# Performance work log

Hardware: AMD Instinct MI355X
Metric: run time of the kernel (lower is better)

The kernel has to match this reference:

```python
import jax, jax.numpy as jnp
import numpy as np

B, N, D, K = 16, 1024, 512, 16  # batch graphs, nodes/graph, feat dim, knn k
NEG_SLOPE = 0.2


def setup_inputs() -> dict:
    key = jax.random.key(0)
    ks = jax.random.split(key, 16)
    s = 1.0 / np.sqrt(D)
    p = {}
    p["x"] = jax.random.normal(ks[0], (B, N, D), dtype=jnp.float32)
    for i, l in enumerate(["1", "2", "3"]):
        p["W" + l] = jax.random.normal(ks[1 + 4 * i], (D, D), dtype=jnp.float32) * s
        p["asrc" + l] = jax.random.normal(ks[2 + 4 * i], (D,), dtype=jnp.float32) * s
        p["adst" + l] = jax.random.normal(ks[3 + 4 * i], (D,), dtype=jnp.float32) * s
        p["b" + l] = jnp.zeros((D,), dtype=jnp.float32)
    p["Wc"] = jax.random.normal(ks[13], (D, 2), dtype=jnp.float32) * s
    p["bc"] = jnp.zeros((2,), dtype=jnp.float32)
    return p


def _knn_idx(pos):
    # pos: [N, D]. k nearest neighbors by euclidean distance, self excluded
    sq = jnp.sum(pos * pos, axis=1)
    d2 = sq[:, None] + sq[None, :] - 2.0 * (pos @ pos.T)  # [N, N]
    d2 = jnp.where(jnp.eye(N, dtype=bool), jnp.inf, d2)
    _, idx = jax.lax.top_k(-d2, K)  # [N, K] neighbor (source) indices per node
    return idx


def _normalize_scale(pos):
    # PyG NormalizeScale: center, then scale so max abs coord ~ 1
    pos = pos - pos.mean(axis=0, keepdims=True)
    return pos * (0.999999 / jnp.max(jnp.abs(pos)))


def _gat(h, nbr, W, asrc, adst, b):
    # GATConv, 1 head, self-loops already included in nbr [N, K+1]
    hp = h @ W                                   # [N, D]
    a_s = hp @ asrc                              # [N] att for sources
    a_d = hp @ adst                              # [N] att for targets
    e = jax.nn.leaky_relu(a_s[nbr] + a_d[:, None], NEG_SLOPE)  # [N, K+1]
    att = jax.nn.softmax(e, axis=-1)             # softmax over each node's in-edges
    msg = hp[nbr]                                # [N, K+1, D] gathered neighbor feats
    return jnp.einsum('nk,nkd->nd', att, msg) + b


def reference(x, W1, asrc1, adst1, b1, W2, asrc2, adst2, b2, W3, asrc3, adst3, b3, Wc, bc):
    self_idx = jnp.arange(N)[:, None]

    def per_graph(pos):
        nbr = jnp.concatenate([_knn_idx(pos), self_idx], axis=1)  # [N, K+1] w/ self-loop
        h = _normalize_scale(pos)
        h = jax.nn.relu(_gat(h, nbr, W1, asrc1, adst1, b1))
        h = jax.nn.relu(_gat(h, nbr, W2, asrc2, adst2, b2))
        h = _gat(h, nbr, W3, asrc3, adst3, b3)
        return h.max(axis=0)  # global max pool over nodes

    g = jax.vmap(per_graph)(x)  # [B, D]
    return g @ Wc + bc          # [B, 2]
```

## Files before the change

### kernel.cpp

```cpp
#include <hip/hip_runtime.h>
#include <hip/hip_bf16.h>
#include <math.h>

#define BATCH 16
#define NNODE 1024
#define DIM   512
#define KNN   16
#define KP1   17
#define NCAND 20
#define NEG   0.2f
#define BT    128
#define NCH   16

typedef __attribute__((ext_vector_type(8))) short bf16x8;
typedef __attribute__((ext_vector_type(4))) float f32x4;

__device__ __forceinline__ unsigned short f2bf(float f) {
    unsigned u = __float_as_uint(f);
    unsigned r = (u + 0x7FFFu + ((u >> 16) & 1u)) >> 16;
    return (unsigned short)r;
}
__device__ __forceinline__ float bf2f(unsigned short h) {
    return __uint_as_float(((unsigned)h) << 16);
}
__device__ __forceinline__ void split_store(float v, unsigned short* hi, unsigned short* lo, size_t idx) {
    unsigned short h = f2bf(v);
    hi[idx] = h;
    lo[idx] = f2bf(v - bf2f(h));
}

__global__ __launch_bounds__(256) void colmean_part(const float* __restrict__ x, float* __restrict__ part) {
    int b = blockIdx.x, dc = blockIdx.y, ch = blockIdx.z;
    int d = dc * 256 + threadIdx.x;
    const float* p = x + ((size_t)b * NNODE + ch * (NNODE / NCH)) * DIM + d;
    float s = 0.f;
    #pragma unroll 4
    for (int n = 0; n < NNODE / NCH; ++n) s += p[(size_t)n * DIM];
    part[((size_t)b * NCH + ch) * DIM + d] = s;
}
__global__ void colmean_fin(const float* __restrict__ part, float* __restrict__ mean) {
    int id = blockIdx.x * 256 + threadIdx.x;
    int b = id >> 9, d = id & (DIM - 1);
    float s = 0.f;
    #pragma unroll
    for (int ch = 0; ch < NCH; ++ch) s += part[((size_t)b * NCH + ch) * DIM + d];
    mean[id] = s * (1.0f / NNODE);
}

__global__ void rowsq_kernel(const float* __restrict__ x, float* __restrict__ sq) {
    int row = blockIdx.x * 4 + (threadIdx.x >> 6);
    int lane = threadIdx.x & 63;
    const float* p = x + (size_t)row * DIM;
    float s = 0.f;
    for (int i = lane; i < DIM; i += 64) { float v = p[i]; s += v * v; }
    #pragma unroll
    for (int off = 32; off > 0; off >>= 1) s += __shfl_down(s, off, 64);
    if (lane == 0) sq[row] = s;
}

__global__ void xtobf_kernel(const float* __restrict__ x, unsigned short* __restrict__ xh) {
    int id = blockIdx.x * 256 + threadIdx.x;
    float4 v = *(const float4*)(x + (size_t)id * 4);
    ushort4 o;
    o.x = f2bf(v.x); o.y = f2bf(v.y); o.z = f2bf(v.z); o.w = f2bf(v.w);
    *(ushort4*)(xh + (size_t)id * 4) = o;
}

__global__ __launch_bounds__(256, 2) void dist_mfma(const unsigned short* __restrict__ xh,
                                                    const float* __restrict__ sq,
                                                    float* __restrict__ d2) {
    __shared__ unsigned short AhL[128][40], BhL[128][40];
    int mt = blockIdx.y;
    int b = mt >> 3;
    int m0 = mt * BT;
    int n0 = blockIdx.x * BT;
    int bn0 = b * NNODE + n0;
    int t = threadIdx.x;
    int lane = t & 63, w = t >> 6;
    int wm = (w >> 1) * 64, wn = (w & 1) * 64;
    int fr = lane & 15, fk = (lane >> 4) * 8;
    f32x4 acc[4][4];
    #pragma unroll
    for (int i = 0; i < 4; ++i)
        #pragma unroll
        for (int j = 0; j < 4; ++j) acc[i][j] = (f32x4){0.f, 0.f, 0.f, 0.f};

    for (int k0 = 0; k0 < DIM; k0 += 32) {
        if (k0) __syncthreads();
        #pragma unroll
        for (int p = 0; p < 2; ++p) {
            int u = t + p * 256;
            int row = u >> 2, seg = (u & 3) * 8;
            *(uint4*)&AhL[row][seg] = *(const uint4*)(xh + (size_t)(m0 + row) * DIM + k0 + seg);
            *(uint4*)&BhL[row][seg] = *(const uint4*)(xh + (size_t)(bn0 + row) * DIM + k0 + seg);
        }
        __syncthreads();
        bf16x8 ah[4], bh[4];
        #pragma unroll
        for (int i = 0; i < 4; ++i) {
            ah[i] = *(const bf16x8*)&AhL[wm + i * 16 + fr][fk];
            bh[i] = *(const bf16x8*)&BhL[wn + i * 16 + fr][fk];
        }
        #pragma unroll
        for (int i = 0; i < 4; ++i)
            #pragma unroll
            for (int j = 0; j < 4; ++j)
                acc[i][j] = __builtin_amdgcn_mfma_f32_16x16x32_bf16(ah[i], bh[j], acc[i][j], 0, 0, 0);
    }
    const float* sqb = sq + b * NNODE;
    int mloc0 = m0 - b * NNODE;
    #pragma unroll
    for (int i = 0; i < 4; ++i) {
        int mloc = mloc0 + wm + i * 16 + (lane >> 4) * 4;
        #pragma unroll
        for (int j = 0; j < 4; ++j) {
            int n = n0 + wn + j * 16 + fr;
            float sqn = sqb[n];
            #pragma unroll
            for (int r = 0; r < 4; ++r) {
                float val = sqb[mloc + r] + sqn - 2.f * acc[i][j][r];
                if (mloc + r == n) val = INFINITY;
                d2[((size_t)b * NNODE + mloc + r) * NNODE + n] = val;
            }
        }
    }
}

__global__ __launch_bounds__(256) void knn_kernel(const float* __restrict__ d2, int* __restrict__ cand) {
    int row = blockIdx.x * 4 + (threadIdx.x >> 6);
    int l = threadIdx.x & 63;
    const float* src = d2 + (size_t)row * NNODE;
    unsigned key[16];
    #pragma unroll
    for (int j = 0; j < 16; ++j) {
        unsigned v = __float_as_uint(src[l + (j << 6)]);
        key[j] = (v & 0xFFFFFC00u) | (unsigned)(l + (j << 6));
    }
    int* dst = cand + row * NCAND;
    unsigned T = 0;
    for (int it = 0; it < NCAND; ++it) {
        unsigned lmin = 0xFFFFFFFFu;
        #pragma unroll
        for (int j = 0; j < 16; ++j) {
            unsigned k = (key[j] > T) ? key[j] : 0xFFFFFFFFu;
            lmin = min(lmin, k);
        }
        #pragma unroll
        for (int off = 1; off < 64; off <<= 1) {
            unsigned o = (unsigned)__shfl_xor((int)lmin, off, 64);
            lmin = min(lmin, o);
        }
        T = lmin;
        if (l == 0) dst[it] = (int)(lmin & 1023u);
    }
}

__global__ __launch_bounds__(256) void rerank_kernel(const float* __restrict__ x,
                                                     const float* __restrict__ sq,
                                                     const int* __restrict__ cand,
                                                     int* __restrict__ nbr) {
    int bid = blockIdx.x;
    int b = bid & (BATCH - 1);
    int w = threadIdx.x >> 6, l = threadIdx.x & 63;
    int m = (bid >> 4) * 4 + w;
    int row = b * NNODE + m;
    const float* xb = x + (size_t)b * NNODE * DIM;
    const float* sqb = sq + b * NNODE;
    const float* xm = xb + (size_t)m * DIM;
    float4 m0v = *(const float4*)(xm + l * 8);
    float4 m1v = *(const float4*)(xm + l * 8 + 4);
    float sqm = sqb[m];

    int idx[NCAND];
    #pragma unroll
    for (int c = 0; c < NCAND; ++c) idx[c] = cand[row * NCAND + c];

    float s[NCAND];
    #pragma unroll
    for (int half = 0; half < 2; ++half) {
        float4 j0[10], j1[10];
        #pragma unroll
        for (int i = 0; i < 10; ++i) {
            const float* xj = xb + (size_t)idx[half * 10 + i] * DIM;
            j0[i] = *(const float4*)(xj + l * 8);
            j1[i] = *(const float4*)(xj + l * 8 + 4);
        }
        #pragma unroll
        for (int i = 0; i < 10; ++i)
            s[half * 10 + i] = m0v.x * j0[i].x + m0v.y * j0[i].y + m0v.z * j0[i].z + m0v.w * j0[i].w
                             + m1v.x * j1[i].x + m1v.y * j1[i].y + m1v.z * j1[i].z + m1v.w * j1[i].w;
    }
    #pragma unroll
    for (int off = 32; off > 0; off >>= 1)
        #pragma unroll
        for (int c = 0; c < NCAND; ++c) s[c] += __shfl_xor(s[c], off, 64);

    unsigned long long key[NCAND];
    #pragma unroll
    for (int c = 0; c < NCAND; ++c) {
        float dv = sqm + sqb[idx[c]] - 2.f * s[c];
        key[c] = ((unsigned long long)__float_as_uint(dv) << 32) | (unsigned)idx[c];
    }
    unsigned long long mykey = ~0ull;
    int myidx = 0;
    #pragma unroll
    for (int c = 0; c < NCAND; ++c) {
        if (l == c) { mykey = key[c]; myidx = idx[c]; }
    }
    int rank = 0;
    #pragma unroll
    for (int c = 0; c < NCAND; ++c) rank += (key[c] < mykey) ? 1 : 0;

    int* dst = nbr + row * KP1;
    if (l < NCAND && rank < KNN) dst[rank] = myidx;
    if (l == 0) dst[KNN] = m;
}

__global__ void init_maxabs(unsigned* maxabs) { if (threadIdx.x < BATCH) maxabs[threadIdx.x] = 0u; }

__global__ __launch_bounds__(256) void maxabs_kernel(const float* __restrict__ x,
                                                     const float* __restrict__ mean,
                                                     unsigned* __restrict__ maxabs) {
    int b = blockIdx.y;
    const float* p = x + ((size_t)b * NNODE + blockIdx.x * 64) * DIM;
    const float* mb = mean + b * DIM;
    float m = 0.f;
    for (int i = threadIdx.x; i < 64 * DIM; i += 256) {
        int d = i & (DIM - 1);
        m = fmaxf(m, fabsf(p[i] - mb[d]));
    }
    __shared__ float red[256];
    red[threadIdx.x] = m; __syncthreads();
    for (int s = 128; s > 0; s >>= 1) {
        if (threadIdx.x < s) red[threadIdx.x] = fmaxf(red[threadIdx.x], red[threadIdx.x + s]);
        __syncthreads();
    }
    if (threadIdx.x == 0) atomicMax(maxabs + b, __float_as_uint(red[0]));
}

__global__ void normalize_kernel(const float* __restrict__ x, const float* __restrict__ mean,
                                 const unsigned* __restrict__ maxabs,
                                 unsigned short* __restrict__ h_hi, unsigned short* __restrict__ h_lo) {
    int id = blockIdx.x * 256 + threadIdx.x;
    int b = id >> 19;
    int d = id & (DIM - 1);
    float scale = 0.999999f / __uint_as_float(maxabs[b]);
    float v = (x[id] - mean[b * DIM + d]) * scale;
    split_store(v, h_hi, h_lo, id);
}

__global__ void wsplit_kernel(const float* __restrict__ W,
                              unsigned short* __restrict__ Wh, unsigned short* __restrict__ Wl) {
    __shared__ float tile[32][33];
    int bx = blockIdx.x * 32, by = blockIdx.y * 32;
    int tx = threadIdx.x & 31, ty = threadIdx.x >> 5;
    #pragma unroll
    for (int i = 0; i < 4; ++i)
        tile[ty + i * 8][tx] = W[(size_t)(by + ty + i * 8) * DIM + bx + tx];
    __syncthreads();
    #pragma unroll
    for (int i = 0; i < 4; ++i) {
        int n = bx + ty + i * 8;
        float v = tile[tx][ty + i * 8];
        split_store(v, Wh, Wl, (size_t)n * DIM + by + tx);
    }
}

__global__ __launch_bounds__(256, 2) void gemm_mfma(const unsigned short* __restrict__ Agh,
                                                    const unsigned short* __restrict__ Agl,
                                                    const unsigned short* __restrict__ Bgh,
                                                    const unsigned short* __restrict__ Bgl,
                                                    float* __restrict__ C) {
    __shared__ unsigned short AhL[128][40], AlL[128][40], BhL[128][40], BlL[128][40];
    int m0 = blockIdx.y * BT, n0 = blockIdx.x * BT;
    int t = threadIdx.x;
    int lane = t & 63, w = t >> 6;
    int wm = (w >> 1) * 64, wn = (w & 1) * 64;
    int fr = lane & 15, fk = (lane >> 4) * 8;
    f32x4 acc[4][4];
    #pragma unroll
    for (int i = 0; i < 4; ++i)
        #pragma unroll
        for (int j = 0; j < 4; ++j) acc[i][j] = (f32x4){0.f, 0.f, 0.f, 0.f};

    for (int k0 = 0; k0 < DIM; k0 += 32) {
        if (k0) __syncthreads();
        #pragma unroll
        for (int p = 0; p < 2; ++p) {
            int u = t + p * 256;
            int row = u >> 2, seg = (u & 3) * 8;
            *(uint4*)&AhL[row][seg] = *(const uint4*)(Agh + (size_t)(m0 + row) * DIM + k0 + seg);
            *(uint4*)&AlL[row][seg] = *(const uint4*)(Agl + (size_t)(m0 + row) * DIM + k0 + seg);
            *(uint4*)&BhL[row][seg] = *(const uint4*)(Bgh + (size_t)(n0 + row) * DIM + k0 + seg);
            *(uint4*)&BlL[row][seg] = *(const uint4*)(Bgl + (size_t)(n0 + row) * DIM + k0 + seg);
        }
        __syncthreads();
        bf16x8 ah[4], al[4], bh[4], bl[4];
        #pragma unroll
        for (int i = 0; i < 4; ++i) {
            ah[i] = *(const bf16x8*)&AhL[wm + i * 16 + fr][fk];
            al[i] = *(const bf16x8*)&AlL[wm + i * 16 + fr][fk];
            bh[i] = *(const bf16x8*)&BhL[wn + i * 16 + fr][fk];
            bl[i] = *(const bf16x8*)&BlL[wn + i * 16 + fr][fk];
        }
        #pragma unroll
        for (int i = 0; i < 4; ++i)
            #pragma unroll
            for (int j = 0; j < 4; ++j) {
                acc[i][j] = __builtin_amdgcn_mfma_f32_16x16x32_bf16(ah[i], bh[j], acc[i][j], 0, 0, 0);
                acc[i][j] = __builtin_amdgcn_mfma_f32_16x16x32_bf16(ah[i], bl[j], acc[i][j], 0, 0, 0);
                acc[i][j] = __builtin_amdgcn_mfma_f32_16x16x32_bf16(al[i], bh[j], acc[i][j], 0, 0, 0);
            }
    }
    #pragma unroll
    for (int i = 0; i < 4; ++i) {
        int mrow = m0 + wm + i * 16 + (lane >> 4) * 4;
        #pragma unroll
        for (int j = 0; j < 4; ++j) {
            int col = n0 + wn + j * 16 + fr;
            #pragma unroll
            for (int r = 0; r < 4; ++r)
                C[(size_t)(mrow + r) * DIM + col] = acc[i][j][r];
        }
    }
}

__global__ void attvec_kernel(const float* __restrict__ hp, const float* __restrict__ asrc,
                              const float* __restrict__ adst, float* __restrict__ as_,
                              float* __restrict__ ad_) {
    int row = blockIdx.x * 4 + (threadIdx.x >> 6);
    int lane = threadIdx.x & 63;
    const float4* p = (const float4*)(hp + (size_t)row * DIM);
    const float4* s4 = (const float4*)asrc;
    const float4* d4 = (const float4*)adst;
    float4 a0 = p[lane], a1 = p[lane + 64];
    float4 u0 = s4[lane], u1 = s4[lane + 64];
    float4 v0 = d4[lane], v1 = d4[lane + 64];
    float s = a0.x * u0.x + a0.y * u0.y + a0.z * u0.z + a0.w * u0.w
            + a1.x * u1.x + a1.y * u1.y + a1.z * u1.z + a1.w * u1.w;
    float d = a0.x * v0.x + a0.y * v0.y + a0.z * v0.z + a0.w * v0.w
            + a1.x * v1.x + a1.y * v1.y + a1.z * v1.z + a1.w * v1.w;
    #pragma unroll
    for (int off = 32; off > 0; off >>= 1) { s += __shfl_down(s, off, 64); d += __shfl_down(d, off, 64); }
    if (lane == 0) { as_[row] = s; ad_[row] = d; }
}

template<int RELU, int SPLIT>
__global__ __launch_bounds__(256) void aggr_kernel(const float* __restrict__ hp, const int* __restrict__ nbr,
                                                   const float* __restrict__ as_, const float* __restrict__ ad_,
                                                   const float* __restrict__ bias,
                                                   float* __restrict__ outf,
                                                   unsigned short* __restrict__ oh,
                                                   unsigned short* __restrict__ ol) {
    __shared__ float attL[4][KP1];
    __shared__ int   jjL[4][KP1];
    int bid = blockIdx.x;
    int b = bid & (BATCH - 1);
    int w = threadIdx.x >> 6, l = threadIdx.x & 63;
    int n = (bid >> 4) * 4 + w;
    int id = b * NNODE + n;

    float e = -INFINITY;
    if (l < KP1) {
        int j = nbr[id * KP1 + l];
        jjL[w][l] = j;
        e = as_[b * NNODE + j] + ad_[id];
        e = (e >= 0.f) ? e : NEG * e;
    }
    float mx = e;
    #pragma unroll
    for (int off = 16; off > 0; off >>= 1) mx = fmaxf(mx, __shfl_xor(mx, off, 64));
    float ex = (l < KP1) ? expf(e - mx) : 0.f;
    float sm = ex;
    #pragma unroll
    for (int off = 16; off > 0; off >>= 1) sm += __shfl_xor(sm, off, 64);
    if (l < KP1) attL[w][l] = ex / sm;

    const float* base = hp + (size_t)b * NNODE * DIM;
    int d0 = l * 8;
    const float4* b4 = (const float4*)(bias + d0);
    float4 o0 = b4[0], o1 = b4[1];
    #pragma unroll
    for (int k = 0; k < KP1; ++k) {
        float a = attL[w][k];
        const float* vp = base + (size_t)jjL[w][k] * DIM + d0;
        float4 v0 = *(const float4*)vp;
        float4 v1 = *(const float4*)(vp + 4);
        o0.x += a * v0.x; o0.y += a * v0.y; o0.z += a * v0.z; o0.w += a * v0.w;
        o1.x += a * v1.x; o1.y += a * v1.y; o1.z += a * v1.z; o1.w += a * v1.w;
    }
    if (RELU) {
        o0.x = fmaxf(o0.x, 0.f); o0.y = fmaxf(o0.y, 0.f); o0.z = fmaxf(o0.z, 0.f); o0.w = fmaxf(o0.w, 0.f);
        o1.x = fmaxf(o1.x, 0.f); o1.y = fmaxf(o1.y, 0.f); o1.z = fmaxf(o1.z, 0.f); o1.w = fmaxf(o1.w, 0.f);
    }
    size_t idx = (size_t)id * DIM + d0;
    if (SPLIT) {
        float v[8] = {o0.x, o0.y, o0.z, o0.w, o1.x, o1.y, o1.z, o1.w};
        unsigned hi[4], lo[4];
        #pragma unroll
        for (int i = 0; i < 4; ++i) {
            unsigned short h0 = f2bf(v[2 * i]),     h1 = f2bf(v[2 * i + 1]);
            unsigned short l0 = f2bf(v[2 * i] - bf2f(h0));
            unsigned short l1 = f2bf(v[2 * i + 1] - bf2f(h1));
            hi[i] = (unsigned)h0 | ((unsigned)h1 << 16);
            lo[i] = (unsigned)l0 | ((unsigned)l1 << 16);
        }
        *(uint4*)(oh + idx) = *(uint4*)hi;
        *(uint4*)(ol + idx) = *(uint4*)lo;
    } else {
        *(float4*)(outf + idx) = o0;
        *(float4*)(outf + idx + 4) = o1;
    }
}

__global__ __launch_bounds__(256) void maxpool_part(const float* __restrict__ h, float* __restrict__ part) {
    int b = blockIdx.x, dc = blockIdx.y, ch = blockIdx.z;
    int d = dc * 256 + threadIdx.x;
    const float* p = h + ((size_t)b * NNODE + ch * (NNODE / NCH)) * DIM + d;
    float m = -INFINITY;
    #pragma unroll 4
    for (int n = 0; n < NNODE / NCH; ++n) m = fmaxf(m, p[(size_t)n * DIM]);
    part[((size_t)b * NCH + ch) * DIM + d] = m;
}
__global__ void maxpool_fin(const float* __restrict__ part, float* __restrict__ g) {
    int id = blockIdx.x * 256 + threadIdx.x;
    int b = id >> 9, d = id & (DIM - 1);
    float m = -INFINITY;
    #pragma unroll
    for (int ch = 0; ch < NCH; ++ch) m = fmaxf(m, part[((size_t)b * NCH + ch) * DIM + d]);
    g[id] = m;
}

__global__ void final_kernel(const float* __restrict__ g, const float* __restrict__ Wc,
                             const float* __restrict__ bc, float* __restrict__ out) {
    int b = blockIdx.x, t = threadIdx.x;
    float s0 = 0.f, s1 = 0.f;
    for (int d = t; d < DIM; d += 256) {
        float v = g[b * DIM + d];
        s0 += v * Wc[d * 2 + 0];
        s1 += v * Wc[d * 2 + 1];
    }
    __shared__ float r0[256], r1[256];
    r0[t] = s0; r1[t] = s1; __syncthreads();
    for (int s = 128; s > 0; s >>= 1) {
        if (t < s) { r0[t] += r0[t + s]; r1[t] += r1[t + s]; }
        __syncthreads();
    }
    if (t == 0) { out[b * 2] = r0[0] + bc[0]; out[b * 2 + 1] = r1[0] + bc[1]; }
}

extern "C" void kernel_launch(void* const* d_in, const int* in_sizes, int n_in,
                              void* d_out, int out_size, void* d_ws, size_t ws_size,
                              hipStream_t stream) {
    const float* x     = (const float*)d_in[0];
    const float* W1    = (const float*)d_in[1];
    const float* asrc1 = (const float*)d_in[2];
    const float* adst1 = (const float*)d_in[3];
    const float* b1    = (const float*)d_in[4];
    const float* W2    = (const float*)d_in[5];
    const float* asrc2 = (const float*)d_in[6];
    const float* adst2 = (const float*)d_in[7];
    const float* b2    = (const float*)d_in[8];
    const float* W3    = (const float*)d_in[9];
    const float* asrc3 = (const float*)d_in[10];
    const float* adst3 = (const float*)d_in[11];
    const float* b3    = (const float*)d_in[12];
    const float* Wc    = (const float*)d_in[13];
    const float* bc    = (const float*)d_in[14];
    float* out = (float*)d_out;

    char* ws = (char*)d_ws;
    float*          d2    = (float*)ws;
    float*          hp    = (float*)ws;
    unsigned short* hA_hi = (unsigned short*)(ws + (32ull << 20));
    unsigned short* hA_lo = (unsigned short*)(ws + (48ull << 20));
    unsigned short* xh    = (unsigned short*)(ws + (64ull << 20));
    unsigned short* hB_hi = (unsigned short*)(ws + (64ull << 20));
    unsigned short* hB_lo = (unsigned short*)(ws + (80ull << 20));
    float*          h3    = (float*)(ws + (64ull << 20));
    size_t off = 96ull << 20;
    unsigned short* Wt1h = (unsigned short*)(ws + off); off += (size_t)DIM * DIM * 2;
    unsigned short* Wt1l = (unsigned short*)(ws + off); off += (size_t)DIM * DIM * 2;
    unsigned short* Wt2h = (unsigned short*)(ws + off); off += (size_t)DIM * DIM * 2;
    unsigned short* Wt2l = (unsigned short*)(ws + off); off += (size_t)DIM * DIM * 2;
    unsigned short* Wt3h = (unsigned short*)(ws + off); off += (size_t)DIM * DIM * 2;
    unsigned short* Wt3l = (unsigned short*)(ws + off); off += (size_t)DIM * DIM * 2;
    int*      nbr    = (int*)(ws + off);      off += (size_t)BATCH * NNODE * KP1 * 4;
    int*      cand   = (int*)(ws + off);      off += (size_t)BATCH * NNODE * NCAND * 4;
    float*    sq     = (float*)(ws + off);    off += (size_t)BATCH * NNODE * 4;
    float*    mean   = (float*)(ws + off);    off += (size_t)BATCH * DIM * 4;
    unsigned* maxabs = (unsigned*)(ws + off); off += 256;
    float*    as_    = (float*)(ws + off);    off += (size_t)BATCH * NNODE * 4;
    float*    ad_    = (float*)(ws + off);    off += (size_t)BATCH * NNODE * 4;
    float*    g      = (float*)(ws + off);    off += (size_t)BATCH * DIM * 4;
    float*    part   = (float*)(ws + off);    off += (size_t)BATCH * NCH * DIM * 4;
    (void)ws_size; (void)in_sizes; (void)n_in; (void)out_size;

    const dim3 cgrid(BATCH, DIM / 256, NCH);
    colmean_part<<<cgrid, 256, 0, stream>>>(x, part);
    colmean_fin<<<BATCH * DIM / 256, 256, 0, stream>>>(part, mean);
    rowsq_kernel<<<BATCH * NNODE / 4, 256, 0, stream>>>(x, sq);
    xtobf_kernel<<<BATCH * NNODE * DIM / 1024, 256, 0, stream>>>(x, xh);
    dist_mfma<<<dim3(NNODE / BT, BATCH * NNODE / BT), 256, 0, stream>>>(xh, sq, d2);
    knn_kernel<<<BATCH * NNODE / 4, 256, 0, stream>>>(d2, cand);
    rerank_kernel<<<BATCH * NNODE / 4, 256, 0, stream>>>(x, sq, cand, nbr);
    wsplit_kernel<<<dim3(16, 16), 256, 0, stream>>>(W1, Wt1h, Wt1l);
    wsplit_kernel<<<dim3(16, 16), 256, 0, stream>>>(W2, Wt2h, Wt2l);
    wsplit_kernel<<<dim3(16, 16), 256, 0, stream>>>(W3, Wt3h, Wt3l);
    init_maxabs<<<1, 64, 0, stream>>>(maxabs);
    maxabs_kernel<<<dim3(16, BATCH), 256, 0, stream>>>(x, mean, maxabs);
    normalize_kernel<<<BATCH * NNODE * DIM / 256, 256, 0, stream>>>(x, mean, maxabs, hA_hi, hA_lo);

    const dim3 ggrid(DIM / BT, BATCH * NNODE / BT);
    gemm_mfma<<<ggrid, 256, 0, stream>>>(hA_hi, hA_lo, Wt1h, Wt1l, hp);
    attvec_kernel<<<BATCH * NNODE / 4, 256, 0, stream>>>(hp, asrc1, adst1, as_, ad_);
    aggr_kernel<1, 1><<<BATCH * NNODE / 4, 256, 0, stream>>>(hp, nbr, as_, ad_, b1, nullptr, hB_hi, hB_lo);
    gemm_mfma<<<ggrid, 256, 0, stream>>>(hB_hi, hB_lo, Wt2h, Wt2l, hp);
    attvec_kernel<<<BATCH * NNODE / 4, 256, 0, stream>>>(hp, asrc2, adst2, as_, ad_);
    aggr_kernel<1, 1><<<BATCH * NNODE / 4, 256, 0, stream>>>(hp, nbr, as_, ad_, b2, nullptr, hA_hi, hA_lo);
    gemm_mfma<<<ggrid, 256, 0, stream>>>(hA_hi, hA_lo, Wt3h, Wt3l, hp);
    attvec_kernel<<<BATCH * NNODE / 4, 256, 0, stream>>>(hp, asrc3, adst3, as_, ad_);
    aggr_kernel<0, 0><<<BATCH * NNODE / 4, 256, 0, stream>>>(hp, nbr, as_, ad_, b3, h3, nullptr, nullptr);
    maxpool_part<<<cgrid, 256, 0, stream>>>(h3, part);
    maxpool_fin<<<BATCH * DIM / 256, 256, 0, stream>>>(part, g);
    final_kernel<<<BATCH, 256, 0, stream>>>(g, Wc, bc, out);
}
```

Measured before the change: 422.9 us.

## Fuse small kernels, emit packed knn keys, shrink candidate set, atomic maxpool

```diff
diff --git a/kernel.cpp b/kernel.cpp
--- a/kernel.cpp
+++ b/kernel.cpp
@@ -7,7 +7,7 @@
 #define DIM   512
 #define KNN   16
 #define KP1   17
-#define NCAND 20
+#define NCAND 18
 #define NEG   0.2f
 #define BT    128
 #define NCH   16
@@ -27,6 +27,12 @@
     unsigned short h = f2bf(v);
     hi[idx] = h;
     lo[idx] = f2bf(v - bf2f(h));
+}
+
+__global__ void init_misc(unsigned* __restrict__ maxabs, unsigned* __restrict__ genc) {
+    int gid = blockIdx.x * 256 + threadIdx.x;
+    if (gid < BATCH) maxabs[gid] = 0u;
+    if (gid < BATCH * DIM) genc[gid] = 0u;
 }
 
 __global__ __launch_bounds__(256) void colmean_part(const float* __restrict__ x, float* __restrict__ part) {
@@ -47,28 +53,30 @@
     mean[id] = s * (1.0f / NNODE);
 }
 
-__global__ void rowsq_kernel(const float* __restrict__ x, float* __restrict__ sq) {
+__global__ __launch_bounds__(256) void rowsq_xtobf(const float* __restrict__ x,
+                                                   float* __restrict__ sq,
+                                                   unsigned short* __restrict__ xh) {
     int row = blockIdx.x * 4 + (threadIdx.x >> 6);
-    int lane = threadIdx.x & 63;
-    const float* p = x + (size_t)row * DIM;
-    float s = 0.f;
-    for (int i = lane; i < DIM; i += 64) { float v = p[i]; s += v * v; }
+    int l = threadIdx.x & 63;
+    const float* p = x + (size_t)row * DIM + l * 8;
+    float4 a = *(const float4*)p;
+    float4 b = *(const float4*)(p + 4);
+    float s = a.x * a.x + a.y * a.y + a.z * a.z + a.w * a.w
+            + b.x * b.x + b.y * b.y + b.z * b.z + b.w * b.w;
+    ushort4 ha, hb;
+    ha.x = f2bf(a.x); ha.y = f2bf(a.y); ha.z = f2bf(a.z); ha.w = f2bf(a.w);
+    hb.x = f2bf(b.x); hb.y = f2bf(b.y); hb.z = f2bf(b.z); hb.w = f2bf(b.w);
+    unsigned short* q = xh + (size_t)row * DIM + l * 8;
+    *(ushort4*)q = ha;
+    *(ushort4*)(q + 4) = hb;
     #pragma unroll
     for (int off = 32; off > 0; off >>= 1) s += __shfl_down(s, off, 64);
-    if (lane == 0) sq[row] = s;
-}
-
-__global__ void xtobf_kernel(const float* __restrict__ x, unsigned short* __restrict__ xh) {
-    int id = blockIdx.x * 256 + threadIdx.x;
-    float4 v = *(const float4*)(x + (size_t)id * 4);
-    ushort4 o;
-    o.x = f2bf(v.x); o.y = f2bf(v.y); o.z = f2bf(v.z); o.w = f2bf(v.w);
-    *(ushort4*)(xh + (size_t)id * 4) = o;
+    if (l == 0) sq[row] = s;
 }
 
 __global__ __launch_bounds__(256, 2) void dist_mfma(const unsigned short* __restrict__ xh,
                                                     const float* __restrict__ sq,
-                                                    float* __restrict__ d2) {
+                                                    unsigned* __restrict__ keys) {
     __shared__ unsigned short AhL[128][40], BhL[128][40];
     int mt = blockIdx.y;
     int b = mt >> 3;
@@ -119,23 +127,21 @@
             #pragma unroll
             for (int r = 0; r < 4; ++r) {
                 float val = sqb[mloc + r] + sqn - 2.f * acc[i][j][r];
-                if (mloc + r == n) val = INFINITY;
-                d2[((size_t)b * NNODE + mloc + r) * NNODE + n] = val;
+                unsigned kv = (__float_as_uint(val) & 0xFFFFFC00u) | (unsigned)n;
+                if (mloc + r == n) kv = 0xFFFFFFFFu;
+                keys[((size_t)b * NNODE + mloc + r) * NNODE + n] = kv;
             }
         }
     }
 }
 
-__global__ __launch_bounds__(256) void knn_kernel(const float* __restrict__ d2, int* __restrict__ cand) {
+__global__ __launch_bounds__(256) void knn_kernel(const unsigned* __restrict__ keys, int* __restrict__ cand) {
     int row = blockIdx.x * 4 + (threadIdx.x >> 6);
     int l = threadIdx.x & 63;
-    const float* src = d2 + (size_t)row * NNODE;
+    const unsigned* src = keys + (size_t)row * NNODE;
     unsigned key[16];
     #pragma unroll
-    for (int j = 0; j < 16; ++j) {
-        unsigned v = __float_as_uint(src[l + (j << 6)]);
-        key[j] = (v & 0xFFFFFC00u) | (unsigned)(l + (j << 6));
-    }
+    for (int j = 0; j < 16; ++j) key[j] = src[l + (j << 6)];
     int* dst = cand + row * NCAND;
     unsigned T = 0;
     for (int it = 0; it < NCAND; ++it) {
@@ -177,46 +183,42 @@
 
     float s[NCAND];
     #pragma unroll
-    for (int half = 0; half < 2; ++half) {
-        float4 j0[10], j1[10];
-        #pragma unroll
-        for (int i = 0; i < 10; ++i) {
-            const float* xj = xb + (size_t)idx[half * 10 + i] * DIM;
+    for (int hf = 0; hf < 3; ++hf) {
+        float4 j0[6], j1[6];
+        #pragma unroll
+        for (int i = 0; i < 6; ++i) {
+            const float* xj = xb + (size_t)idx[hf * 6 + i] * DIM;
             j0[i] = *(const float4*)(xj + l * 8);
             j1[i] = *(const float4*)(xj + l * 8 + 4);
         }
         #pragma unroll
-        for (int i = 0; i < 10; ++i)
-            s[half * 10 + i] = m0v.x * j0[i].x + m0v.y * j0[i].y + m0v.z * j0[i].z + m0v.w * j0[i].w
-                             + m1v.x * j1[i].x + m1v.y * j1[i].y + m1v.z * j1[i].z + m1v.w * j1[i].w;
+        for (int i = 0; i < 6; ++i)
+            s[hf * 6 + i] = m0v.x * j0[i].x + m0v.y * j0[i].y + m0v.z * j0[i].z + m0v.w * j0[i].w
+                          + m1v.x * j1[i].x + m1v.y * j1[i].y + m1v.z * j1[i].z + m1v.w * j1[i].w;
     }
     #pragma unroll
     for (int off = 32; off > 0; off >>= 1)
         #pragma unroll
         for (int c = 0; c < NCAND; ++c) s[c] += __shfl_xor(s[c], off, 64);
 
-    unsigned long long key[NCAND];
-    #pragma unroll
-    for (int c = 0; c < NCAND; ++c) {
-        float dv = sqm + sqb[idx[c]] - 2.f * s[c];
-        key[c] = ((unsigned long long)__float_as_uint(dv) << 32) | (unsigned)idx[c];
-    }
-    unsigned long long mykey = ~0ull;
-    int myidx = 0;
-    #pragma unroll
-    for (int c = 0; c < NCAND; ++c) {
-        if (l == c) { mykey = key[c]; myidx = idx[c]; }
-    }
+    float dv[NCAND];
+    #pragma unroll
+    for (int c = 0; c < NCAND; ++c) dv[c] = sqm + sqb[idx[c]] - 2.f * s[c];
+
+    float mydv = 0.f; int myidx = 0;
+    #pragma unroll
+    for (int c = 0; c < NCAND; ++c)
+        if (l == c) { mydv = dv[c]; myidx = idx[c]; }
+
     int rank = 0;
     #pragma unroll
-    for (int c = 0; c < NCAND; ++c) rank += (key[c] < mykey) ? 1 : 0;
+    for (int c = 0; c < NCAND; ++c)
+        rank += (dv[c] < mydv || (dv[c] == mydv && idx[c] < myidx)) ? 1 : 0;
 
     int* dst = nbr + row * KP1;
     if (l < NCAND && rank < KNN) dst[rank] = myidx;
     if (l == 0) dst[KNN] = m;
 }
-
-__global__ void init_maxabs(unsigned* maxabs) { if (threadIdx.x < BATCH) maxabs[threadIdx.x] = 0u; }
 
 __global__ __launch_bounds__(256) void maxabs_kernel(const float* __restrict__ x,
                                                      const float* __restrict__ mean,
@@ -249,8 +251,15 @@
     split_store(v, h_hi, h_lo, id);
 }
 
-__global__ void wsplit_kernel(const float* __restrict__ W,
-                              unsigned short* __restrict__ Wh, unsigned short* __restrict__ Wl) {
+__global__ void wsplit_kernel(const float* __restrict__ W1, const float* __restrict__ W2,
+                              const float* __restrict__ W3,
+                              unsigned short* __restrict__ Wh1, unsigned short* __restrict__ Wl1,
+                              unsigned short* __restrict__ Wh2, unsigned short* __restrict__ Wl2,
+                              unsigned short* __restrict__ Wh3, unsigned short* __restrict__ Wl3) {
+    int z = blockIdx.z;
+    const float* W = (z == 0) ? W1 : (z == 1) ? W2 : W3;
+    unsigned short* Wh = (z == 0) ? Wh1 : (z == 1) ? Wh2 : Wh3;
+    unsigned short* Wl = (z == 0) ? Wl1 : (z == 1) ? Wl2 : Wl3;
     __shared__ float tile[32][33];
     int bx = blockIdx.x * 32, by = blockIdx.y * 32;
     int tx = threadIdx.x & 31, ty = threadIdx.x >> 5;
@@ -413,30 +422,26 @@
     }
 }
 
-__global__ __launch_bounds__(256) void maxpool_part(const float* __restrict__ h, float* __restrict__ part) {
+__global__ __launch_bounds__(256) void maxpool_atomic(const float* __restrict__ h, unsigned* __restrict__ genc) {
     int b = blockIdx.x, dc = blockIdx.y, ch = blockIdx.z;
     int d = dc * 256 + threadIdx.x;
     const float* p = h + ((size_t)b * NNODE + ch * (NNODE / NCH)) * DIM + d;
     float m = -INFINITY;
     #pragma unroll 4
     for (int n = 0; n < NNODE / NCH; ++n) m = fmaxf(m, p[(size_t)n * DIM]);
-    part[((size_t)b * NCH + ch) * DIM + d] = m;
-}
-__global__ void maxpool_fin(const float* __restrict__ part, float* __restrict__ g) {
-    int id = blockIdx.x * 256 + threadIdx.x;
-    int b = id >> 9, d = id & (DIM - 1);
-    float m = -INFINITY;
-    #pragma unroll
-    for (int ch = 0; ch < NCH; ++ch) m = fmaxf(m, part[((size_t)b * NCH + ch) * DIM + d]);
-    g[id] = m;
-}
-
-__global__ void final_kernel(const float* __restrict__ g, const float* __restrict__ Wc,
+    unsigned u = __float_as_uint(m);
+    unsigned enc = (u & 0x80000000u) ? ~u : (u | 0x80000000u);
+    atomicMax(genc + b * DIM + d, enc);
+}
+
+__global__ void final_kernel(const unsigned* __restrict__ genc, const float* __restrict__ Wc,
                              const float* __restrict__ bc, float* __restrict__ out) {
     int b = blockIdx.x, t = threadIdx.x;
     float s0 = 0.f, s1 = 0.f;
     for (int d = t; d < DIM; d += 256) {
-        float v = g[b * DIM + d];
+        unsigned e = genc[b * DIM + d];
+        unsigned u = (e & 0x80000000u) ? (e ^ 0x80000000u) : ~e;
+        float v = __uint_as_float(u);
         s0 += v * Wc[d * 2 + 0];
         s1 += v * Wc[d * 2 + 1];
     }
@@ -470,7 +475,7 @@
     float* out = (float*)d_out;
 
     char* ws = (char*)d_ws;
-    float*          d2    = (float*)ws;
+    unsigned*       keys  = (unsigned*)ws;
     float*          hp    = (float*)ws;
     unsigned short* hA_hi = (unsigned short*)(ws + (32ull << 20));
     unsigned short* hA_lo = (unsigned short*)(ws + (48ull << 20));
@@ -492,22 +497,19 @@
     unsigned* maxabs = (unsigned*)(ws + off); off += 256;
     float*    as_    = (float*)(ws + off);    off += (size_t)BATCH * NNODE * 4;
     float*    ad_    = (float*)(ws + off);    off += (size_t)BATCH * NNODE * 4;
-    float*    g      = (float*)(ws + off);    off += (size_t)BATCH * DIM * 4;
+    unsigned* genc   = (unsigned*)(ws + off); off += (size_t)BATCH * DIM * 4;
     float*    part   = (float*)(ws + off);    off += (size_t)BATCH * NCH * DIM * 4;
     (void)ws_size; (void)in_sizes; (void)n_in; (void)out_size;
 
     const dim3 cgrid(BATCH, DIM / 256, NCH);
+    init_misc<<<32, 256, 0, stream>>>(maxabs, genc);
     colmean_part<<<cgrid, 256, 0, stream>>>(x, part);
     colmean_fin<<<BATCH * DIM / 256, 256, 0, stream>>>(part, mean);
-    rowsq_kernel<<<BATCH * NNODE / 4, 256, 0, stream>>>(x, sq);
-    xtobf_kernel<<<BATCH * NNODE * DIM / 1024, 256, 0, stream>>>(x, xh);
-    dist_mfma<<<dim3(NNODE / BT, BATCH * NNODE / BT), 256, 0, stream>>>(xh, sq, d2);
-    knn_kernel<<<BATCH * NNODE / 4, 256, 0, stream>>>(d2, cand);
+    rowsq_xtobf<<<BATCH * NNODE / 4, 256, 0, stream>>>(x, sq, xh);
+    dist_mfma<<<dim3(NNODE / BT, BATCH * NNODE / BT), 256, 0, stream>>>(xh, sq, keys);
+    knn_kernel<<<BATCH * NNODE / 4, 256, 0, stream>>>(keys, cand);
     rerank_kernel<<<BATCH * NNODE / 4, 256, 0, stream>>>(x, sq, cand, nbr);
-    wsplit_kernel<<<dim3(16, 16), 256, 0, stream>>>(W1, Wt1h, Wt1l);
-    wsplit_kernel<<<dim3(16, 16), 256, 0, stream>>>(W2, Wt2h, Wt2l);
-    wsplit_kernel<<<dim3(16, 16), 256, 0, stream>>>(W3, Wt3h, Wt3l);
-    init_maxabs<<<1, 64, 0, stream>>>(maxabs);
+    wsplit_kernel<<<dim3(16, 16, 3), 256, 0, stream>>>(W1, W2, W3, Wt1h, Wt1l, Wt2h, Wt2l, Wt3h, Wt3l);
     maxabs_kernel<<<dim3(16, BATCH), 256, 0, stream>>>(x, mean, maxabs);
     normalize_kernel<<<BATCH * NNODE * DIM / 256, 256, 0, stream>>>(x, mean, maxabs, hA_hi, hA_lo);
 
@@ -521,7 +523,6 @@
     gemm_mfma<<<ggrid, 256, 0, stream>>>(hA_hi, hA_lo, Wt3h, Wt3l, hp);
     attvec_kernel<<<BATCH * NNODE / 4, 256, 0, stream>>>(hp, asrc3, adst3, as_, ad_);
     aggr_kernel<0, 0><<<BATCH * NNODE / 4, 256, 0, stream>>>(hp, nbr, as_, ad_, b3, h3, nullptr, nullptr);
-    maxpool_part<<<cgrid, 256, 0, stream>>>(h3, part);
-    maxpool_fin<<<BATCH * DIM / 256, 256, 0, stream>>>(part, g);
-    final_kernel<<<BATCH, 256, 0, stream>>>(g, Wc, bc, out);
-}
+    maxpool_atomic<<<cgrid, 256, 0, stream>>>(h3, genc);
+    final_kernel<<<BATCH, 256, 0, stream>>>(genc, Wc, bc, out);
+}
```

Measured after the change: 422.6 us. Within noise of the previous version (-0.1%).
